# Kernel optimization log

Hardware: AMD Instinct MI355X
Metric: run time of the kernel (lower is better)

The kernel has to match this reference:

```python
import jax, jax.numpy as jnp
import numpy as np

EPS = 1e-5

def setup_inputs() -> dict:
    key = jax.random.key(0)
    ks = jax.random.split(key, 9)
    N, D, L, C = 1, 128, 256, 256
    OC, PC = 32, 256
    msa_matrix = jax.random.normal(ks[0], (N, D, L, C), dtype=jnp.float32)
    ln_w = jnp.ones((C,), dtype=jnp.float32)
    ln_b = jnp.zeros((C,), dtype=jnp.float32)
    s = 1.0 / np.sqrt(C)
    Wl = jax.random.uniform(ks[1], (OC, C), dtype=jnp.float32, minval=-s, maxval=s)
    bl = jax.random.uniform(ks[2], (OC,), dtype=jnp.float32, minval=-s, maxval=s)
    Wr = jax.random.uniform(ks[3], (OC, C), dtype=jnp.float32, minval=-s, maxval=s)
    br = jax.random.uniform(ks[4], (OC,), dtype=jnp.float32, minval=-s, maxval=s)
    so = 1.0 / np.sqrt(OC * OC)
    Wout = jax.random.uniform(ks[5], (PC, OC * OC), dtype=jnp.float32, minval=-so, maxval=so)
    bout = jax.random.uniform(ks[6], (PC,), dtype=jnp.float32, minval=-so, maxval=so)
    return {"msa_matrix": msa_matrix, "ln_w": ln_w, "ln_b": ln_b,
            "Wl": Wl, "bl": bl, "Wr": Wr, "br": br, "Wout": Wout, "bout": bout}

def reference(msa_matrix, ln_w, ln_b, Wl, bl, Wr, br, Wout, bout):
    N, D, L, C = msa_matrix.shape
    OC = Wl.shape[0]
    # LayerNorm over channels
    mu = jnp.mean(msa_matrix, axis=-1, keepdims=True)
    var = jnp.var(msa_matrix, axis=-1, keepdims=True)
    x = (msa_matrix - mu) * jax.lax.rsqrt(var + EPS) * ln_w + ln_b
    # Dual projections: [N, D, L, OC]
    left = jnp.einsum('ndlc,oc->ndlo', x, Wl) + bl
    right = (jnp.einsum('ndlc,oc->ndlo', x, Wr) + br) / D
    # Outer-product mean over MSA depth: [N, L, L, OC, OC]
    outprod = jnp.einsum('ndlc,ndmq->nlmcq', left, right)
    outprod = outprod.reshape(N, L, L, OC * OC)
    # Output projection to pair channels
    return jnp.einsum('nlmk,pk->nlmp', outprod, Wout) + bout
```

## Files before the change

kernel.cpp:

```cpp
#include <hip/hip_runtime.h>

#define EPS 1e-5f

static constexpr int D  = 128;
static constexpr int L  = 256;
static constexpr int C  = 256;
static constexpr int OC = 32;
static constexpr int PC = 256;

typedef __attribute__((ext_vector_type(8))) short bfrag8;
typedef __attribute__((ext_vector_type(4))) short bhalf4;
typedef __attribute__((ext_vector_type(4))) float f32x4;
typedef __attribute__((ext_vector_type(4))) unsigned int u32x4;

__device__ inline unsigned short f2bf(float f) {
  union { float f; unsigned u; } v; v.f = f;
  unsigned r = v.u + 0x7FFF + ((v.u >> 16) & 1);
  return (unsigned short)(r >> 16);
}

__global__ __launch_bounds__(256)
void prep(const float* __restrict__ Wl, const float* __restrict__ Wr,
          const float* __restrict__ Wout,
          unsigned short* __restrict__ Wbf3, unsigned short* __restrict__ Wlnf) {
  const int t = threadIdx.x, b = blockIdx.x;
  {
    const int e0 = (b * 256 + t) * 4;
    const int lane = (e0 >> 3) & 63, ks = (e0 >> 9) & 31, pf = e0 >> 14;
    const int p = pf * 16 + (lane & 15);
    unsigned short v[4];
    #pragma unroll
    for (int j = 0; j < 4; ++j) {
      const int kp = ks * 32 + ((lane >> 4) * 8) + ((e0 + j) & 7);
      const int c = kp & 31, q = kp >> 5;
      v[j] = f2bf(Wout[p * 1024 + c * 32 + q]);
    }
    *(bhalf4*)(Wbf3 + e0) = *(bhalf4*)v;
  }
  if (b < 16) {
    const int e0 = (b * 256 + t) * 4;
    const int lane = (e0 >> 3) & 63, ks = (e0 >> 9) & 7, nf = e0 >> 12;
    const int n = nf * 16 + (lane & 15);
    unsigned short v[4];
    #pragma unroll
    for (int j = 0; j < 4; ++j) {
      const int k = ks * 32 + ((lane >> 4) * 8) + ((e0 + j) & 7);
      v[j] = f2bf(n < 32 ? Wl[n * 256 + k] : Wr[(n - 32) * 256 + k]);
    }
    *(bhalf4*)(Wlnf + e0) = *(bhalf4*)v;
  }
}

__global__ __launch_bounds__(256, 4)
void ln_proj(const float* __restrict__ msa,
             const float* __restrict__ lnw, const float* __restrict__ lnb,
             const unsigned short* __restrict__ Wlnf,
             const float* __restrict__ bl, const float* __restrict__ br,
             unsigned short* __restrict__ leftT, unsigned short* __restrict__ rightT) {
  __shared__ char xb[32768];

  const int t = threadIdx.x, lane = t & 63, w = t >> 6;
  const int d0 = blockIdx.x * 8, l0 = blockIdx.y * 8;

  float4 xv[16];
  #pragma unroll
  for (int i = 0; i < 16; ++i) {
    const int r = i * 4 + w, dd = r & 7, ll = r >> 3;
    xv[i] = *(const float4*)(msa + ((size_t)(d0 + dd) * 256 + (l0 + ll)) * 256 + lane * 4);
  }

  float mu[16], rs[16];
  #pragma unroll
  for (int i = 0; i < 16; ++i) {
    float s  = xv[i].x + xv[i].y + xv[i].z + xv[i].w;
    float s2 = xv[i].x * xv[i].x + xv[i].y * xv[i].y + xv[i].z * xv[i].z + xv[i].w * xv[i].w;
    #pragma unroll
    for (int off = 32; off >= 1; off >>= 1) {
      s  += __shfl_xor(s, off);
      s2 += __shfl_xor(s2, off);
    }
    mu[i] = s * (1.0f / C);
    rs[i] = rsqrtf(s2 * (1.0f / C) - mu[i] * mu[i] + EPS);
  }

  {
    const float4 wv = *(const float4*)(lnw + lane * 4);
    const float4 bv = *(const float4*)(lnb + lane * 4);
    #pragma unroll
    for (int i = 0; i < 16; ++i) {
      const int r = i * 4 + w;
      float4 v = xv[i];
      unsigned short u[4];
      u[0] = f2bf((v.x - mu[i]) * rs[i] * wv.x + bv.x);
      u[1] = f2bf((v.y - mu[i]) * rs[i] * wv.y + bv.y);
      u[2] = f2bf((v.z - mu[i]) * rs[i] * wv.z + bv.z);
      u[3] = f2bf((v.w - mu[i]) * rs[i] * wv.w + bv.w);
      *(bhalf4*)&xb[r * 512 + ((lane * 8) ^ ((r & 7) << 4))] = *(bhalf4*)u;
    }
  }
  __syncthreads();

  bfrag8 wf[8];
  {
    const unsigned short* Wp = Wlnf + ((size_t)w * 8 * 64 + lane) * 8;
    #pragma unroll
    for (int ks = 0; ks < 8; ++ks) wf[ks] = *(const bfrag8*)(Wp + ks * 512);
  }
  f32x4 acc[4];
  #pragma unroll
  for (int mf = 0; mf < 4; ++mf) acc[mf] = (f32x4)0.f;
  #pragma unroll
  for (int ks = 0; ks < 8; ++ks) {
    #pragma unroll
    for (int mf = 0; mf < 4; ++mf) {
      const int row = mf * 16 + (lane & 15);
      const bfrag8 af = *(const bfrag8*)&xb[row * 512 +
                          ((ks * 64 + ((lane >> 4) << 4)) ^ ((row & 7) << 4))];
      acc[mf] = __builtin_amdgcn_mfma_f32_16x16x32_bf16(af, wf[ks], acc[mf], 0, 0, 0);
    }
  }

  {
    const int n = w * 16 + (lane & 15);
    const int side = n >> 5, o = n & 31;
    const float bias = side ? br[o] : bl[o];
    const float sc = side ? (1.0f / D) : 1.0f;
    unsigned short* dst = side ? rightT : leftT;
    #pragma unroll
    for (int mf = 0; mf < 4; ++mf) {
      const int rbase = mf * 16 + ((lane >> 4) << 2);
      const int ll = rbase >> 3, ddb = rbase & 7;
      unsigned short u[4];
      #pragma unroll
      for (int r = 0; r < 4; ++r) u[r] = f2bf((acc[mf][r] + bias) * sc);
      *(bhalf4*)(dst + ((size_t)(l0 + ll) * 32 + o) * 128 + d0 + ddb) = *(bhalf4*)u;
    }
  }
}

__global__ __launch_bounds__(512, 4)
void fused_mfma(const unsigned short* __restrict__ leftT,
                const unsigned short* __restrict__ rightT,
                const unsigned short* __restrict__ Wbf3,
                const float* __restrict__ bout,
                float* __restrict__ out) {
  __shared__ char smem[65536];

  const int flat = blockIdx.x;
  const int wg = (flat & 7) * 256 + (flat >> 3);
  const int mt = wg & 31, lt = wg >> 5;
  const int l0 = lt * 4, m0 = mt * 8;

  const char* Aslab = (const char*)(leftT  + (size_t)l0 * 32 * 128);
  const char* Bslab = (const char*)(rightT + (size_t)m0 * 32 * 128);

  const int tid = threadIdx.x, lane = tid & 63, w = tid >> 6;
  const int wr = w >> 2, wc = w & 3;

  f32x4 acc[4][4];
  #pragma unroll
  for (int i = 0; i < 4; ++i)
    #pragma unroll
    for (int j = 0; j < 4; ++j) acc[i][j] = (f32x4)0.f;

  auto stageA = [&](int kh, int dst) {
    #pragma unroll
    for (int i = 0; i < 2; ++i) {
      const int lb = (i * 512 + tid) * 16;
      const int row = lb >> 7;
      const int sb = (lb & 127) ^ ((row & 7) << 4);
      __builtin_amdgcn_global_load_lds((const void*)(Aslab + (size_t)row * 256 + kh * 128 + sb),
                                       (void*)&smem[dst + lb], 16, 0, 0);
    }
  };
  auto stageB = [&](int kh) {
    #pragma unroll
    for (int i = 0; i < 4; ++i) {
      const int lb = (i * 512 + tid) * 16;
      const int row = lb >> 7;
      const int sb = (lb & 127) ^ ((row & 7) << 4);
      __builtin_amdgcn_global_load_lds((const void*)(Bslab + (size_t)row * 256 + kh * 128 + sb),
                                       (void*)&smem[16384 + lb], 16, 0, 0);
    }
  };
  auto computeKh = [&](int abase) {
    #pragma unroll
    for (int ks = 0; ks < 2; ++ks) {
      const int kb = ks * 64 + ((lane >> 4) << 4);
      bfrag8 a[4], b[4];
      #pragma unroll
      for (int i = 0; i < 4; ++i) {
        const int row = wr * 64 + i * 16 + (lane & 15);
        a[i] = *(const bfrag8*)&smem[abase + (row << 7) + (kb ^ ((row & 7) << 4))];
      }
      #pragma unroll
      for (int j = 0; j < 4; ++j) {
        const int row = wc * 64 + j * 16 + (lane & 15);
        b[j] = *(const bfrag8*)&smem[16384 + (row << 7) + (kb ^ ((row & 7) << 4))];
      }
      #pragma unroll
      for (int i = 0; i < 4; ++i)
        #pragma unroll
        for (int j = 0; j < 4; ++j)
          acc[i][j] = __builtin_amdgcn_mfma_f32_16x16x32_bf16(a[i], b[j], acc[i][j], 0, 0, 0);
    }
  };

  stageA(0, 0);
  stageB(0);
  __syncthreads();
  stageA(1, 49152);
  u32x4 b1r[4];
  #pragma unroll
  for (int i = 0; i < 4; ++i) {
    const int lb = (i * 512 + tid) * 16;
    const int row = lb >> 7;
    const int sb = (lb & 127) ^ ((row & 7) << 4);
    b1r[i] = *(const u32x4*)(Bslab + (size_t)row * 256 + 128 + sb);
  }
  computeKh(0);
  __syncthreads();
  #pragma unroll
  for (int i = 0; i < 4; ++i)
    *(u32x4*)&smem[16384 + (i * 512 + tid) * 16] = b1r[i];
  __syncthreads();
  computeKh(49152);
  __syncthreads();

  {
    #pragma unroll
    for (int i = 0; i < 4; ++i) {
      const int rowb = wr * 64 + i * 16 + ((lane >> 4) << 2);
      const int ll = rowb >> 5, cc = rowb & 31;
      #pragma unroll
      for (int j = 0; j < 4; ++j) {
        const int col = wc * 64 + j * 16 + (lane & 15);
        const int mm = col >> 5, q = col & 31;
        const int pair = ll * 8 + mm;
        const int kp = q * 32 + cc;
        const int S = (pair & 7) ^ ((q >> 1) & 7);
        const int byte = pair * 2048 + ((kp * 2) ^ (S << 4));
        uint2 u;
        u.x = (unsigned)f2bf(acc[i][j][0]) | ((unsigned)f2bf(acc[i][j][1]) << 16);
        u.y = (unsigned)f2bf(acc[i][j][2]) | ((unsigned)f2bf(acc[i][j][3]) << 16);
        *(uint2*)&smem[byte] = u;
      }
    }
  }

  const unsigned short* wp0 = Wbf3 + (((size_t)(w * 2)     * 32) * 64 + lane) * 8;
  const unsigned short* wp1 = Wbf3 + (((size_t)(w * 2 + 1) * 32) * 64 + lane) * 8;

  bfrag8 wfs[4][2];
  #pragma unroll
  for (int s = 0; s < 4; ++s) {
    wfs[s][0] = *(const bfrag8*)(wp0 + s * 512);
    wfs[s][1] = *(const bfrag8*)(wp1 + s * 512);
  }
  __syncthreads();

  f32x4 oacc[2][2];
  #pragma unroll
  for (int u = 0; u < 2; ++u)
    #pragma unroll
    for (int pj = 0; pj < 2; ++pj) oacc[u][pj] = (f32x4)0.f;

  auto ldos = [&](int ks, bfrag8* o) {
    #pragma unroll
    for (int pj = 0; pj < 2; ++pj) {
      const int pair = pj * 16 + (lane & 15);
      const int S = (pair & 7) ^ ((ks >> 1) & 7);
      o[pj] = *(const bfrag8*)&smem[pair * 2048 + ((ks * 64 + ((lane >> 4) << 4)) ^ (S << 4))];
    }
  };

  bfrag8 osA[2], osB[2];
  ldos(0, osA);

  #pragma unroll
  for (int ks = 0; ks < 32; ks += 2) {
    ldos(ks + 1, osB);
    __builtin_amdgcn_s_setprio(1);
    oacc[0][0] = __builtin_amdgcn_mfma_f32_16x16x32_bf16(wfs[ks & 3][0], osA[0], oacc[0][0], 0, 0, 0);
    oacc[0][1] = __builtin_amdgcn_mfma_f32_16x16x32_bf16(wfs[ks & 3][0], osA[1], oacc[0][1], 0, 0, 0);
    oacc[1][0] = __builtin_amdgcn_mfma_f32_16x16x32_bf16(wfs[ks & 3][1], osA[0], oacc[1][0], 0, 0, 0);
    oacc[1][1] = __builtin_amdgcn_mfma_f32_16x16x32_bf16(wfs[ks & 3][1], osA[1], oacc[1][1], 0, 0, 0);
    __builtin_amdgcn_s_setprio(0);
    if (ks + 4 < 32) {
      wfs[ks & 3][0] = *(const bfrag8*)(wp0 + (ks + 4) * 512);
      wfs[ks & 3][1] = *(const bfrag8*)(wp1 + (ks + 4) * 512);
    }
    if (ks + 2 < 32) ldos(ks + 2, osA);
    __builtin_amdgcn_s_setprio(1);
    oacc[0][0] = __builtin_amdgcn_mfma_f32_16x16x32_bf16(wfs[(ks + 1) & 3][0], osB[0], oacc[0][0], 0, 0, 0);
    oacc[0][1] = __builtin_amdgcn_mfma_f32_16x16x32_bf16(wfs[(ks + 1) & 3][0], osB[1], oacc[0][1], 0, 0, 0);
    oacc[1][0] = __builtin_amdgcn_mfma_f32_16x16x32_bf16(wfs[(ks + 1) & 3][1], osB[0], oacc[1][0], 0, 0, 0);
    oacc[1][1] = __builtin_amdgcn_mfma_f32_16x16x32_bf16(wfs[(ks + 1) & 3][1], osB[1], oacc[1][1], 0, 0, 0);
    __builtin_amdgcn_s_setprio(0);
    if (ks + 5 < 32) {
      wfs[(ks + 1) & 3][0] = *(const bfrag8*)(wp0 + (ks + 5) * 512);
      wfs[(ks + 1) & 3][1] = *(const bfrag8*)(wp1 + (ks + 5) * 512);
    }
  }

  {
    #pragma unroll
    for (int u = 0; u < 2; ++u) {
      const int p0 = (w * 2 + u) * 16 + ((lane >> 4) << 2);
      const float4 bb = *(const float4*)&bout[p0];
      #pragma unroll
      for (int pj = 0; pj < 2; ++pj) {
        const int pair = pj * 16 + (lane & 15);
        const int ll = pair >> 3, mm = pair & 7;
        float4 v;
        v.x = oacc[u][pj][0] + bb.x;
        v.y = oacc[u][pj][1] + bb.y;
        v.z = oacc[u][pj][2] + bb.z;
        v.w = oacc[u][pj][3] + bb.w;
        *(float4*)&out[((size_t)(l0 + ll) * L + (m0 + mm)) * PC + p0] = v;
      }
    }
  }
}

extern "C" void kernel_launch(void* const* d_in, const int* in_sizes, int n_in,
                              void* d_out, int out_size, void* d_ws, size_t ws_size,
                              hipStream_t stream) {
  const float* msa  = (const float*)d_in[0];
  const float* ln_w = (const float*)d_in[1];
  const float* ln_b = (const float*)d_in[2];
  const float* Wl   = (const float*)d_in[3];
  const float* bl   = (const float*)d_in[4];
  const float* Wr   = (const float*)d_in[5];
  const float* br   = (const float*)d_in[6];
  const float* Wout = (const float*)d_in[7];
  const float* bout = (const float*)d_in[8];
  float* out = (float*)d_out;

  unsigned short* leftT  = (unsigned short*)d_ws;
  unsigned short* rightT = leftT + (size_t)L * 32 * 128;
  unsigned short* Wbf3   = rightT + (size_t)L * 32 * 128;
  unsigned short* Wlnf   = Wbf3 + (size_t)PC * 1024;

  prep<<<dim3(256), 256, 0, stream>>>(Wl, Wr, Wout, Wbf3, Wlnf);
  ln_proj<<<dim3(16, 32), 256, 0, stream>>>(msa, ln_w, ln_b, Wlnf, bl, br, leftT, rightT);
  fused_mfma<<<dim3(2048), 512, 0, stream>>>(leftT, rightT, Wbf3, bout, out);
}
```

Measured before the change: 84.18 us.

## Split fused outer-product/projection kernel into two kernels via global bf16 intermediate

When the workspace is large enough, the fused kernel is replaced by two kernels. op_outer computes per-tile outer products and writes them to global memory in bf16, in a swizzled layout suited to MFMA. op_proj then runs the output projection GEMM over that buffer with higher per-wave reuse of the weights. This is meant to relieve register and LDS pressure in the fused kernel and simplify the projection loop. The cost is a large intermediate buffer that must round-trip through HBM.

```diff
diff --git a/kernel.cpp b/kernel.cpp
--- a/kernel.cpp
+++ b/kernel.cpp
@@ -134,6 +134,186 @@
       #pragma unroll
       for (int r = 0; r < 4; ++r) u[r] = f2bf((acc[mf][r] + bias) * sc);
       *(bhalf4*)(dst + ((size_t)(l0 + ll) * 32 + o) * 128 + d0 + ddb) = *(bhalf4*)u;
+    }
+  }
+}
+
+__global__ __launch_bounds__(512, 4)
+void op_outer(const unsigned short* __restrict__ leftT,
+              const unsigned short* __restrict__ rightT,
+              unsigned short* __restrict__ OsG) {
+  __shared__ char smem[65536];
+
+  const int flat = blockIdx.x;
+  const int wg = (flat & 7) * 256 + (flat >> 3);
+  const int mt = wg & 31, lt = wg >> 5;
+  const int l0 = lt * 4, m0 = mt * 8;
+
+  const char* Aslab = (const char*)(leftT  + (size_t)l0 * 32 * 128);
+  const char* Bslab = (const char*)(rightT + (size_t)m0 * 32 * 128);
+
+  const int tid = threadIdx.x, lane = tid & 63, w = tid >> 6;
+  const int wr = w >> 2, wc = w & 3;
+
+  f32x4 acc[4][4];
+  #pragma unroll
+  for (int i = 0; i < 4; ++i)
+    #pragma unroll
+    for (int j = 0; j < 4; ++j) acc[i][j] = (f32x4)0.f;
+
+  auto stageA = [&](int kh, int dst) {
+    #pragma unroll
+    for (int i = 0; i < 2; ++i) {
+      const int lb = (i * 512 + tid) * 16;
+      const int row = lb >> 7;
+      const int sb = (lb & 127) ^ ((row & 7) << 4);
+      __builtin_amdgcn_global_load_lds((const void*)(Aslab + (size_t)row * 256 + kh * 128 + sb),
+                                       (void*)&smem[dst + lb], 16, 0, 0);
+    }
+  };
+  auto stageB = [&](int kh) {
+    #pragma unroll
+    for (int i = 0; i < 4; ++i) {
+      const int lb = (i * 512 + tid) * 16;
+      const int row = lb >> 7;
+      const int sb = (lb & 127) ^ ((row & 7) << 4);
+      __builtin_amdgcn_global_load_lds((const void*)(Bslab + (size_t)row * 256 + kh * 128 + sb),
+                                       (void*)&smem[16384 + lb], 16, 0, 0);
+    }
+  };
+  auto computeKh = [&](int abase) {
+    #pragma unroll
+    for (int ks = 0; ks < 2; ++ks) {
+      const int kb = ks * 64 + ((lane >> 4) << 4);
+      bfrag8 a[4], b[4];
+      #pragma unroll
+      for (int i = 0; i < 4; ++i) {
+        const int row = wr * 64 + i * 16 + (lane & 15);
+        a[i] = *(const bfrag8*)&smem[abase + (row << 7) + (kb ^ ((row & 7) << 4))];
+      }
+      #pragma unroll
+      for (int j = 0; j < 4; ++j) {
+        const int row = wc * 64 + j * 16 + (lane & 15);
+        b[j] = *(const bfrag8*)&smem[16384 + (row << 7) + (kb ^ ((row & 7) << 4))];
+      }
+      #pragma unroll
+      for (int i = 0; i < 4; ++i)
+        #pragma unroll
+        for (int j = 0; j < 4; ++j)
+          acc[i][j] = __builtin_amdgcn_mfma_f32_16x16x32_bf16(a[i], b[j], acc[i][j], 0, 0, 0);
+    }
+  };
+
+  stageA(0, 0);
+  stageB(0);
+  __syncthreads();
+  stageA(1, 49152);
+  u32x4 b1r[4];
+  #pragma unroll
+  for (int i = 0; i < 4; ++i) {
+    const int lb = (i * 512 + tid) * 16;
+    const int row = lb >> 7;
+    const int sb = (lb & 127) ^ ((row & 7) << 4);
+    b1r[i] = *(const u32x4*)(Bslab + (size_t)row * 256 + 128 + sb);
+  }
+  computeKh(0);
+  __syncthreads();
+  #pragma unroll
+  for (int i = 0; i < 4; ++i)
+    *(u32x4*)&smem[16384 + (i * 512 + tid) * 16] = b1r[i];
+  __syncthreads();
+  computeKh(49152);
+  __syncthreads();
+
+  {
+    #pragma unroll
+    for (int i = 0; i < 4; ++i) {
+      const int rowb = wr * 64 + i * 16 + ((lane >> 4) << 2);
+      const int ll = rowb >> 5, cc = rowb & 31;
+      #pragma unroll
+      for (int j = 0; j < 4; ++j) {
+        const int col = wc * 64 + j * 16 + (lane & 15);
+        const int mm = col >> 5, q = col & 31;
+        const int pair = ll * 8 + mm;
+        const int kp = q * 32 + cc;
+        const int S = (pair & 7) ^ ((q >> 1) & 7);
+        const int byte = pair * 2048 + ((kp * 2) ^ (S << 4));
+        uint2 u;
+        u.x = (unsigned)f2bf(acc[i][j][0]) | ((unsigned)f2bf(acc[i][j][1]) << 16);
+        u.y = (unsigned)f2bf(acc[i][j][2]) | ((unsigned)f2bf(acc[i][j][3]) << 16);
+        *(uint2*)&smem[byte] = u;
+      }
+    }
+  }
+  __syncthreads();
+
+  {
+    char* dst = (char*)OsG + (size_t)flat * 65536;
+    #pragma unroll
+    for (int s = 0; s < 8; ++s) {
+      const int e0 = (s * 512 + tid) * 8;
+      const int nf = e0 >> 14, ks = (e0 >> 9) & 31, l6 = (e0 >> 3) & 63;
+      const int pair = nf * 16 + (l6 & 15);
+      const int kpb = ks * 32 + ((l6 >> 4) << 3);
+      const int S = (pair & 7) ^ ((kpb >> 6) & 7);
+      const bfrag8 v = *(const bfrag8*)&smem[pair * 2048 + ((kpb * 2) ^ (S << 4))];
+      *(bfrag8*)(dst + (size_t)e0 * 2) = v;
+    }
+  }
+}
+
+__global__ __launch_bounds__(512, 4)
+void op_proj(const unsigned short* __restrict__ OsG,
+             const unsigned short* __restrict__ Wbf3,
+             const float* __restrict__ bout,
+             float* __restrict__ out) {
+  const int b = blockIdx.x;
+  const int tid = threadIdx.x, lane = tid & 63, w = tid >> 6;
+  const int wr = w >> 1, wc = w & 1;
+
+  const unsigned short* afp = Wbf3 + (size_t)wr * 4 * 16384 + (size_t)lane * 8;
+  const unsigned short* bfp = OsG + ((size_t)(4 * b + wc * 2)) * 32768 + (size_t)lane * 8;
+
+  f32x4 acc[4][4];
+  #pragma unroll
+  for (int i = 0; i < 4; ++i)
+    #pragma unroll
+    for (int n = 0; n < 4; ++n) acc[i][n] = (f32x4)0.f;
+
+  #pragma unroll 4
+  for (int ks = 0; ks < 32; ++ks) {
+    bfrag8 af[4], bf[4];
+    #pragma unroll
+    for (int i = 0; i < 4; ++i)
+      af[i] = *(const bfrag8*)(afp + (size_t)i * 16384 + ks * 512);
+    #pragma unroll
+    for (int n = 0; n < 4; ++n)
+      bf[n] = *(const bfrag8*)(bfp + (size_t)(n >> 1) * 32768 + (n & 1) * 16384 + ks * 512);
+    #pragma unroll
+    for (int i = 0; i < 4; ++i)
+      #pragma unroll
+      for (int n = 0; n < 4; ++n)
+        acc[i][n] = __builtin_amdgcn_mfma_f32_16x16x32_bf16(af[i], bf[n], acc[i][n], 0, 0, 0);
+  }
+
+  #pragma unroll
+  for (int n = 0; n < 4; ++n) {
+    const int chunkFlat = 4 * b + wc * 2 + (n >> 1);
+    const int cwg = (chunkFlat & 7) * 256 + (chunkFlat >> 3);
+    const int mt = cwg & 31, lt = cwg >> 5;
+    const int pairLoc = (n & 1) * 16 + (lane & 15);
+    const int ll = pairLoc >> 3, mm = pairLoc & 7;
+    const size_t rowbase = ((size_t)(lt * 4 + ll) * L + (mt * 8 + mm)) * PC;
+    #pragma unroll
+    for (int i = 0; i < 4; ++i) {
+      const int p0 = (wr * 4 + i) * 16 + ((lane >> 4) << 2);
+      const float4 bb = *(const float4*)&bout[p0];
+      float4 v;
+      v.x = acc[i][n][0] + bb.x;
+      v.y = acc[i][n][1] + bb.y;
+      v.z = acc[i][n][2] + bb.z;
+      v.w = acc[i][n][3] + bb.w;
+      *(float4*)&out[rowbase + p0] = v;
     }
   }
 }
@@ -341,8 +521,16 @@
   unsigned short* rightT = leftT + (size_t)L * 32 * 128;
   unsigned short* Wbf3   = rightT + (size_t)L * 32 * 128;
   unsigned short* Wlnf   = Wbf3 + (size_t)PC * 1024;
+  unsigned short* OsG    = Wlnf + 16384;
+
+  const size_t ws_needed = ((char*)(OsG + (size_t)2048 * 32768) - (char*)d_ws);
 
   prep<<<dim3(256), 256, 0, stream>>>(Wl, Wr, Wout, Wbf3, Wlnf);
   ln_proj<<<dim3(16, 32), 256, 0, stream>>>(msa, ln_w, ln_b, Wlnf, bl, br, leftT, rightT);
-  fused_mfma<<<dim3(2048), 512, 0, stream>>>(leftT, rightT, Wbf3, bout, out);
-}
+  if (ws_size >= ws_needed) {
+    op_outer<<<dim3(2048), 512, 0, stream>>>(leftT, rightT, OsG);
+    op_proj<<<dim3(512), 512, 0, stream>>>(OsG, Wbf3, bout, out);
+  } else {
+    fused_mfma<<<dim3(2048), 512, 0, stream>>>(leftT, rightT, Wbf3, bout, out);
+  }
+}
```

Result: slower. 112.5 us (+33.6%).
